# Performance work log

Hardware: AMD Instinct MI355X
Metric: run time of the kernel (lower is better)

## Reference

```python
import jax, jax.numpy as jnp
import numpy as np
import math

N_HEAD = 16
DEG = 2
EPS = 1e-7


def setup_inputs() -> dict:
    key = jax.random.key(0)
    k1, k2 = jax.random.split(key)
    B, T, C = 2, 2048, 1024
    x = jax.random.normal(k1, (B, T, C), dtype=jnp.float32)
    W = jax.random.normal(k2, (3 * C + N_HEAD, C), dtype=jnp.float32) * (1.0 / math.sqrt(C))
    return {"x": x, "W": W}


def reference(x, W):
    # JacobAttentionLayer.forward with attention_kernel='powerref' (AttentionReference,
    # deg=2, scale=1/sqrt(hs), eps=1e-7, log-space power softmax, gating=True).
    B, T, C = x.shape
    nh = N_HEAD
    hs = C // nh
    scale = 1.0 / math.sqrt(hs)

    qkvgr = jnp.einsum('btc,oc->bto', x, W)  # [B,T,3C+nh]
    q, k, v = (qkvgr[..., :C], qkvgr[..., C:2 * C], qkvgr[..., 2 * C:3 * C])
    log_g = jax.nn.log_sigmoid(qkvgr[..., 3 * C:].astype(jnp.float32))  # [B,T,nh]
    log_G = jnp.cumsum(log_g, axis=1).transpose(0, 2, 1)  # [B,nh,T]

    def heads(a):  # [B,T,C] -> [B,nh,T,hs]
        return a.reshape(B, T, nh, hs).transpose(0, 2, 1, 3)

    Q, K, V = heads(q), heads(k), heads(v)

    S = jnp.einsum('bhtd,bhsd->bhts', Q, K)  # [B,nh,T,T]
    # log-space power attention: deg*log(|S|+eps) + log(scale) + gating
    Tm = DEG * jnp.log(jnp.abs(S) + EPS) + jnp.log(jnp.float32(scale))
    Z = Tm + log_G[..., :, None] - log_G[..., None, :]
    mask = jnp.tril(jnp.ones((T, T), dtype=bool))
    Z = jnp.where(mask, Z, -jnp.inf)
    Z_rowmax = jax.lax.stop_gradient(jnp.max(Z, axis=-1, keepdims=True))
    P = jnp.exp(Z - Z_rowmax)  # deg even -> no sign correction

    norm = jnp.sum(P, axis=-1)  # [B,nh,T]
    O = jnp.einsum('bhts,bhsd->bhtd', P, V)
    y = O / norm[..., None]
    return y.transpose(0, 2, 1, 3).reshape(B, T, C)
```

## Files before the change

### kernel.cpp

```cpp
#include <hip/hip_runtime.h>
#include <math.h>

typedef __attribute__((ext_vector_type(4))) float f32x4;
typedef __attribute__((ext_vector_type(8))) short short8;

#define NEG_INF (-__builtin_inff())

__device__ __forceinline__ unsigned short f2bf(float f) {
    union { float f; unsigned u; } v; v.f = f;
    unsigned r = v.u + 0x7FFFu + ((v.u >> 16) & 1u);
    return (unsigned short)(r >> 16);
}
__device__ __forceinline__ float bf2f(unsigned short h) {
    union { unsigned u; float f; } v; v.u = ((unsigned)h) << 16;
    return v.f;
}

__device__ __forceinline__ f32x4 mfma_bf16(short8 a, short8 b, f32x4 c) {
    return __builtin_amdgcn_mfma_f32_16x16x32_bf16(a, b, c, 0, 0, 0);
}

__device__ __forceinline__ void gload_lds16(const unsigned short* g, unsigned short* l) {
    __builtin_amdgcn_global_load_lds(
        (const __attribute__((address_space(1))) void*)g,
        (__attribute__((address_space(3))) void*)l, 16, 0, 0);
}

__global__ void split_kernel(const float* __restrict__ in,
                             unsigned short* __restrict__ hi,
                             unsigned short* __restrict__ lo, int n4)
{
    int i = blockIdx.x * 256 + threadIdx.x;
    if (i >= n4) return;
    float4 v = ((const float4*)in)[i];
    ushort4 h, l;
    h.x = f2bf(v.x); l.x = f2bf(v.x - bf2f(h.x));
    h.y = f2bf(v.y); l.y = f2bf(v.y - bf2f(h.y));
    h.z = f2bf(v.z); l.z = f2bf(v.z - bf2f(h.z));
    h.w = f2bf(v.w); l.w = f2bf(v.w - bf2f(h.w));
    ((ushort4*)hi)[i] = h;
    ((ushort4*)lo)[i] = l;
}

__global__ __launch_bounds__(256, 3)
void gemm_proj(const unsigned short* __restrict__ xh, const unsigned short* __restrict__ xl,
               const unsigned short* __restrict__ wh, const unsigned short* __restrict__ wl,
               unsigned short* __restrict__ Qh, unsigned short* __restrict__ Ql,
               unsigned short* __restrict__ Kh, unsigned short* __restrict__ Kl,
               unsigned short* __restrict__ Vtg, float* __restrict__ gbuf)
{
    __shared__ __align__(16) unsigned short Ah[128][32];
    __shared__ __align__(16) unsigned short Al[128][32];
    __shared__ __align__(16) unsigned short Bh[128][32];
    __shared__ __align__(16) unsigned short Bl[128][32];

    const int mt = blockIdx.x & 31;
    const int nt = blockIdx.x >> 5;
    const int m0 = mt * 128, n0 = nt * 128;
    const int tid = threadIdx.x;
    const int w = tid >> 6, l = tid & 63;
    const int wm = w >> 1, wn = w & 1;
    const int lr = l & 15, lq = l >> 4;
    const int xs = (lr >> 1) & 3;
    const bool needLo = (nt < 16) || (nt == 24);

    f32x4 acc[4][4];
#pragma unroll
    for (int i = 0; i < 4; ++i)
#pragma unroll
        for (int j = 0; j < 4; ++j) acc[i][j] = (f32x4){0.f, 0.f, 0.f, 0.f};

    const int srow = tid >> 2;
    const int sp = tid & 3;

    for (int k0 = 0; k0 < 1024; k0 += 32) {
        __syncthreads();
#pragma unroll
        for (int p = 0; p < 2; ++p) {
            int r = srow + p * 64;
            int sc = (sp ^ ((r >> 1) & 3)) * 8;
            int o = n0 + r;
            int oc = o < 3088 ? o : 3087;
            gload_lds16(&xh[(size_t)(m0 + r) * 1024 + k0 + sc], &Ah[r][sp * 8]);
            gload_lds16(&wh[(size_t)oc * 1024 + k0 + sc],       &Bh[r][sp * 8]);
            if (needLo) {
                gload_lds16(&xl[(size_t)(m0 + r) * 1024 + k0 + sc], &Al[r][sp * 8]);
                gload_lds16(&wl[(size_t)oc * 1024 + k0 + sc],       &Bl[r][sp * 8]);
            }
        }
        __asm__ volatile("s_waitcnt vmcnt(0)" ::: "memory");
        __syncthreads();

        short8 ah[4], bh4[4], al4[4], bl4[4];
#pragma unroll
        for (int i = 0; i < 4; ++i) {
            ah[i]  = *(const short8*)&Ah[wm * 64 + i * 16 + lr][(lq ^ xs) * 8];
            bh4[i] = *(const short8*)&Bh[wn * 64 + i * 16 + lr][(lq ^ xs) * 8];
        }
        if (needLo) {
#pragma unroll
            for (int i = 0; i < 4; ++i) {
                al4[i] = *(const short8*)&Al[wm * 64 + i * 16 + lr][(lq ^ xs) * 8];
                bl4[i] = *(const short8*)&Bl[wn * 64 + i * 16 + lr][(lq ^ xs) * 8];
            }
        }
#pragma unroll
        for (int i = 0; i < 4; ++i)
#pragma unroll
            for (int j = 0; j < 4; ++j) {
                acc[i][j] = mfma_bf16(ah[i], bh4[j], acc[i][j]);
                if (needLo) {
                    acc[i][j] = mfma_bf16(ah[i], bl4[j], acc[i][j]);
                    acc[i][j] = mfma_bf16(al4[i], bh4[j], acc[i][j]);
                }
            }
    }

#pragma unroll
    for (int i = 0; i < 4; ++i) {
        int nrow0 = m0 + wm * 64 + i * 16 + lq * 4;
        int b = nrow0 >> 11;
        int tbase = nrow0 & 2047;
#pragma unroll
        for (int j = 0; j < 4; ++j) {
            int o = n0 + wn * 64 + j * 16 + lr;
            if (o < 1024) {
                int h = o >> 6, d = o & 63;
                size_t base = ((size_t)(b * 16 + h) * 2048 + tbase) * 64 + d;
#pragma unroll
                for (int r = 0; r < 4; ++r) {
                    float v = acc[i][j][r];
                    unsigned short hi_ = f2bf(v);
                    unsigned short lo_ = f2bf(v - bf2f(hi_));
                    Qh[base + (size_t)r * 64] = hi_;
                    Ql[base + (size_t)r * 64] = lo_;
                }
            } else if (o < 2048) {
                int oo = o - 1024;
                int h = oo >> 6, d = oo & 63;
                size_t base = ((size_t)(b * 16 + h) * 2048 + tbase) * 64 + d;
#pragma unroll
                for (int r = 0; r < 4; ++r) {
                    float v = acc[i][j][r];
                    unsigned short hi_ = f2bf(v);
                    unsigned short lo_ = f2bf(v - bf2f(hi_));
                    Kh[base + (size_t)r * 64] = hi_;
                    Kl[base + (size_t)r * 64] = lo_;
                }
            } else if (o < 3072) {
                int oo = o - 2048;
                int h = oo >> 6, d = oo & 63;
                size_t base = ((size_t)(b * 16 + h) * 64 + d) * 2048 + tbase;
                ushort4 pk;
                pk.x = f2bf(acc[i][j][0]);
                pk.y = f2bf(acc[i][j][1]);
                pk.z = f2bf(acc[i][j][2]);
                pk.w = f2bf(acc[i][j][3]);
                *(ushort4*)&Vtg[base] = pk;
            } else if (o < 3088) {
                int og = o - 3072;
#pragma unroll
                for (int r = 0; r < 4; ++r)
                    gbuf[(size_t)(nrow0 + r) * 16 + og] = acc[i][j][r];
            }
        }
    }
}

__global__ void gate_scan(const float* __restrict__ g, float* __restrict__ lg)
{
    const int bh = blockIdx.x;
    const int b = bh >> 4, h = bh & 15;
    const int tid = threadIdx.x;
    __shared__ float part[256];

    float vals[8];
    float run = 0.f;
#pragma unroll
    for (int j = 0; j < 8; ++j) {
        int t = tid * 8 + j;
        float x = g[(size_t)(b * 2048 + t) * 16 + h];
        float ls = fminf(x, 0.f) - log1pf(__expf(-fabsf(x)));
        run += ls * 1.4426950408889634f;
        vals[j] = run;
    }
    part[tid] = run;
    __syncthreads();
    for (int ofs = 1; ofs < 256; ofs <<= 1) {
        float add = (tid >= ofs) ? part[tid - ofs] : 0.f;
        __syncthreads();
        part[tid] += add;
        __syncthreads();
    }
    float excl = part[tid] - run;
#pragma unroll
    for (int j = 0; j < 8; ++j)
        lg[(size_t)bh * 2048 + tid * 8 + j] = excl + vals[j];
}

__global__ __launch_bounds__(256, 3)
void attn_fwd(const unsigned short* __restrict__ Qh, const unsigned short* __restrict__ Ql,
              const unsigned short* __restrict__ Kh, const unsigned short* __restrict__ Kl,
              const unsigned short* __restrict__ Vtg, const float* __restrict__ lg,
              float* __restrict__ out)
{
    __shared__ __align__(16) unsigned short kh[64][64];
    __shared__ __align__(16) unsigned short kl[64][64];
    __shared__ __align__(16) unsigned short vs[64][64];
    __shared__ __align__(16) unsigned short pl[4][16][64];

    const int bid = blockIdx.x;
    const int qi = (bid & 7) | ((bid >> 8) << 3);
    const int bh = (bid >> 3) & 31;
    const int tid = threadIdx.x;
    const int w = tid >> 6, l = tid & 63;
    const int lr = l & 15, lq = l >> 4;
    const int xk = lr & 7;
    const int q0 = qi * 64;
    const int myrow0 = q0 + w * 16;

    const size_t qoff = ((size_t)bh * 2048 + myrow0 + lr) * 64;
    short8 qh8[2], ql8[2];
    qh8[0] = *(const short8*)&Qh[qoff + lq * 8];
    qh8[1] = *(const short8*)&Qh[qoff + 32 + lq * 8];
    ql8[0] = *(const short8*)&Ql[qoff + lq * 8];
    ql8[1] = *(const short8*)&Ql[qoff + 32 + lq * 8];

    float gq2[4];
#pragma unroll
    for (int r = 0; r < 4; ++r)
        gq2[r] = lg[(size_t)bh * 2048 + myrow0 + lq * 4 + r] - 3.0f;

    float M_[4]  = {0.f, 0.f, 0.f, 0.f};
    float ls_[4] = {0.f, 0.f, 0.f, 0.f};
    f32x4 o4[4];
#pragma unroll
    for (int i = 0; i < 4; ++i) o4[i] = (f32x4){0.f, 0.f, 0.f, 0.f};

    const int srow = tid >> 3;
    const int schunk = tid & 7;

    const unsigned short* Kh_b = Kh + (size_t)bh * 2048 * 64;
    const unsigned short* Kl_b = Kl + (size_t)bh * 2048 * 64;
    const unsigned short* Vt_b = Vtg + (size_t)bh * 64 * 2048;

    for (int kv0 = 0; kv0 <= q0; kv0 += 64) {
        __syncthreads();
#pragma unroll
        for (int p = 0; p < 2; ++p) {
            int r = srow + p * 32;
            int sc = (schunk ^ (r & 7)) * 8;
            gload_lds16(&Kh_b[(size_t)(kv0 + r) * 64 + sc], &kh[r][schunk * 8]);
            gload_lds16(&Kl_b[(size_t)(kv0 + r) * 64 + sc], &kl[r][schunk * 8]);
            gload_lds16(&Vt_b[(size_t)r * 2048 + kv0 + sc], &vs[r][schunk * 8]);
        }
        __asm__ volatile("s_waitcnt vmcnt(0)" ::: "memory");
        __syncthreads();

        float gsl[4];
#pragma unroll
        for (int js = 0; js < 4; ++js)
            gsl[js] = lg[(size_t)bh * 2048 + kv0 + js * 16 + lr];

        f32x4 sa[4];
#pragma unroll
        for (int js = 0; js < 4; ++js) sa[js] = (f32x4){0.f, 0.f, 0.f, 0.f};
#pragma unroll
        for (int js = 0; js < 4; ++js)
#pragma unroll
            for (int ks = 0; ks < 2; ++ks) {
                short8 kb  = *(const short8*)&kh[js * 16 + lr][((ks * 4 + lq) ^ xk) << 3];
                short8 kbl = *(const short8*)&kl[js * 16 + lr][((ks * 4 + lq) ^ xk) << 3];
                sa[js] = mfma_bf16(qh8[ks], kb,  sa[js]);
                sa[js] = mfma_bf16(qh8[ks], kbl, sa[js]);
                sa[js] = mfma_bf16(ql8[ks], kb,  sa[js]);
            }

        const bool diag = (kv0 == q0);
#pragma unroll
        for (int js = 0; js < 4; ++js) {
            float ga = gsl[js];
#pragma unroll
            for (int r = 0; r < 4; ++r) {
                float a = fabsf(sa[js][r]) + 1e-7f;
                float ex = exp2f(gq2[r] - ga);
                float wv = a * a * ex;
                if (diag && (js * 16 + lr > w * 16 + lq * 4 + r)) wv = 0.f;
                sa[js][r] = wv;
            }
        }

        float f_[4], rMv[4];
#pragma unroll
        for (int r = 0; r < 4; ++r) {
            float a = fmaxf(fmaxf(sa[0][r], sa[1][r]), fmaxf(sa[2][r], sa[3][r]));
#pragma unroll
            for (int msk = 1; msk < 16; msk <<= 1)
                a = fmaxf(a, __shfl_xor(a, msk, 16));
            float Mn = fmaxf(M_[r], a);
            bool pos = Mn > 1e-30f;
            float rM = pos ? __builtin_amdgcn_rcpf(Mn) : 0.f;
            f_[r]  = pos ? M_[r] * rM : 1.f;
            rMv[r] = rM;
            M_[r]  = Mn;
        }

        float rs_[4] = {0.f, 0.f, 0.f, 0.f};
#pragma unroll
        for (int js = 0; js < 4; ++js)
#pragma unroll
            for (int r = 0; r < 4; ++r) {
                float pv = sa[js][r] * rMv[r];
                sa[js][r] = pv;
                rs_[r] += pv;
            }
#pragma unroll
        for (int r = 0; r < 4; ++r) {
            float s = rs_[r];
#pragma unroll
            for (int msk = 1; msk < 16; msk <<= 1)
                s += __shfl_xor(s, msk, 16);
            ls_[r] = ls_[r] * f_[r] + s;
        }
#pragma unroll
        for (int ds_ = 0; ds_ < 4; ++ds_)
#pragma unroll
            for (int r = 0; r < 4; ++r)
                o4[ds_][r] *= f_[r];

#pragma unroll
        for (int js = 0; js < 4; ++js)
#pragma unroll
            for (int r = 0; r < 4; ++r) {
                int prow = lq * 4 + r;
                int cch = (js * 2 + (lr >> 3)) ^ (prow & 7);
                pl[w][prow][(cch << 3) | (lr & 7)] = f2bf(sa[js][r]);
            }
        __asm__ volatile("s_waitcnt lgkmcnt(0)" ::: "memory");
        __builtin_amdgcn_sched_barrier(0);

        short8 pa0 = *(const short8*)&pl[w][lr][((0 + lq) ^ xk) << 3];
        short8 pa1 = *(const short8*)&pl[w][lr][((4 + lq) ^ xk) << 3];
#pragma unroll
        for (int ds_ = 0; ds_ < 4; ++ds_) {
            short8 vb0 = *(const short8*)&vs[ds_ * 16 + lr][((0 + lq) ^ xk) << 3];
            short8 vb1 = *(const short8*)&vs[ds_ * 16 + lr][((4 + lq) ^ xk) << 3];
            o4[ds_] = mfma_bf16(pa0, vb0, o4[ds_]);
            o4[ds_] = mfma_bf16(pa1, vb1, o4[ds_]);
        }
    }

    const int b = bh >> 4, h = bh & 15;
#pragma unroll
    for (int ds_ = 0; ds_ < 4; ++ds_)
#pragma unroll
        for (int r = 0; r < 4; ++r) {
            int t = myrow0 + lq * 4 + r;
            out[(size_t)(b * 2048 + t) * 1024 + h * 64 + ds_ * 16 + lr] =
                o4[ds_][r] / ls_[r];
        }
}

extern "C" void kernel_launch(void* const* d_in, const int* in_sizes, int n_in,
                              void* d_out, int out_size, void* d_ws, size_t ws_size,
                              hipStream_t stream)
{
    const float* x = (const float*)d_in[0];
    const float* W = (const float*)d_in[1];
    float* out = (float*)d_out;

    const size_t NX = 4194304;
    const size_t NW = 3162112;
    const size_t NQ = 4194304;

    char* ws = (char*)d_ws;
    size_t off = 0;
    auto alloc = [&](size_t bytes) -> void* {
        void* p = ws + off;
        off += (bytes + 255) & ~(size_t)255;
        return p;
    };
    unsigned short* xh = (unsigned short*)alloc(NX * 2);
    unsigned short* xl = (unsigned short*)alloc(NX * 2);
    unsigned short* wh = (unsigned short*)alloc(NW * 2);
    unsigned short* wl = (unsigned short*)alloc(NW * 2);
    unsigned short* Qh = (unsigned short*)alloc(NQ * 2);
    unsigned short* Ql = (unsigned short*)alloc(NQ * 2);
    unsigned short* Kh = (unsigned short*)alloc(NQ * 2);
    unsigned short* Kl = (unsigned short*)alloc(NQ * 2);
    unsigned short* Vt = (unsigned short*)alloc(NQ * 2);
    float* g  = (float*)alloc(65536 * 4);
    float* lg = (float*)alloc(65536 * 4);
    if (off > ws_size) return;

    split_kernel<<<(int)(NX / 4 + 255) / 256, 256, 0, stream>>>(x, xh, xl, (int)(NX / 4));
    split_kernel<<<(int)(NW / 4 + 255) / 256, 256, 0, stream>>>(W, wh, wl, (int)(NW / 4));
    gemm_proj<<<800, 256, 0, stream>>>(xh, xl, wh, wl, Qh, Ql, Kh, Kl, Vt, g);
    gate_scan<<<32, 256, 0, stream>>>(g, lg);
    attn_fwd<<<1024, 256, 0, stream>>>(Qh, Ql, Kh, Kl, Vt, lg, out);
}
```

Before: 213.6 us.

## Double-buffer LDS tiles in projection GEMM and attention, reverse KV order with lazy rescale

Both the projection GEMM and the attention kernel now use two LDS buffers, so the global-to-LDS load of the next tile is issued before computing on the current one. This hides memory latency behind MFMA work. The attention kernel also walks KV tiles from the diagonal backwards and skips the running-max rescale of the output and normaliser unless some row's max grows. The cost is twice the shared memory and occupancy lowered from 3 to 2 blocks per CU.

```diff
diff --git a/kernel.cpp b/kernel.cpp
--- a/kernel.cpp
+++ b/kernel.cpp
@@ -42,17 +42,17 @@
     ((ushort4*)lo)[i] = l;
 }
 
-__global__ __launch_bounds__(256, 3)
+__global__ __launch_bounds__(256, 2)
 void gemm_proj(const unsigned short* __restrict__ xh, const unsigned short* __restrict__ xl,
                const unsigned short* __restrict__ wh, const unsigned short* __restrict__ wl,
                unsigned short* __restrict__ Qh, unsigned short* __restrict__ Ql,
                unsigned short* __restrict__ Kh, unsigned short* __restrict__ Kl,
                unsigned short* __restrict__ Vtg, float* __restrict__ gbuf)
 {
-    __shared__ __align__(16) unsigned short Ah[128][32];
-    __shared__ __align__(16) unsigned short Al[128][32];
-    __shared__ __align__(16) unsigned short Bh[128][32];
-    __shared__ __align__(16) unsigned short Bl[128][32];
+    __shared__ __align__(16) unsigned short Ah[2][128][32];
+    __shared__ __align__(16) unsigned short Al[2][128][32];
+    __shared__ __align__(16) unsigned short Bh[2][128][32];
+    __shared__ __align__(16) unsigned short Bl[2][128][32];
 
     const int mt = blockIdx.x & 31;
     const int nt = blockIdx.x >> 5;
@@ -73,35 +73,41 @@
     const int srow = tid >> 2;
     const int sp = tid & 3;
 
-    for (int k0 = 0; k0 < 1024; k0 += 32) {
-        __syncthreads();
+    auto STAGE = [&](int bsel, int k0) {
 #pragma unroll
         for (int p = 0; p < 2; ++p) {
             int r = srow + p * 64;
             int sc = (sp ^ ((r >> 1) & 3)) * 8;
             int o = n0 + r;
             int oc = o < 3088 ? o : 3087;
-            gload_lds16(&xh[(size_t)(m0 + r) * 1024 + k0 + sc], &Ah[r][sp * 8]);
-            gload_lds16(&wh[(size_t)oc * 1024 + k0 + sc],       &Bh[r][sp * 8]);
+            gload_lds16(&xh[(size_t)(m0 + r) * 1024 + k0 + sc], &Ah[bsel][r][sp * 8]);
+            gload_lds16(&wh[(size_t)oc * 1024 + k0 + sc],       &Bh[bsel][r][sp * 8]);
             if (needLo) {
-                gload_lds16(&xl[(size_t)(m0 + r) * 1024 + k0 + sc], &Al[r][sp * 8]);
-                gload_lds16(&wl[(size_t)oc * 1024 + k0 + sc],       &Bl[r][sp * 8]);
-            }
-        }
-        __asm__ volatile("s_waitcnt vmcnt(0)" ::: "memory");
-        __syncthreads();
+                gload_lds16(&xl[(size_t)(m0 + r) * 1024 + k0 + sc], &Al[bsel][r][sp * 8]);
+                gload_lds16(&wl[(size_t)oc * 1024 + k0 + sc],       &Bl[bsel][r][sp * 8]);
+            }
+        }
+    };
+
+    STAGE(0, 0);
+    __asm__ volatile("s_waitcnt vmcnt(0)" ::: "memory");
+    __syncthreads();
+
+    int cur = 0;
+    for (int k0 = 0; k0 < 1024; k0 += 32) {
+        if (k0 + 32 < 1024) STAGE(cur ^ 1, k0 + 32);
 
         short8 ah[4], bh4[4], al4[4], bl4[4];
 #pragma unroll
         for (int i = 0; i < 4; ++i) {
-            ah[i]  = *(const short8*)&Ah[wm * 64 + i * 16 + lr][(lq ^ xs) * 8];
-            bh4[i] = *(const short8*)&Bh[wn * 64 + i * 16 + lr][(lq ^ xs) * 8];
+            ah[i]  = *(const short8*)&Ah[cur][wm * 64 + i * 16 + lr][(lq ^ xs) * 8];
+            bh4[i] = *(const short8*)&Bh[cur][wn * 64 + i * 16 + lr][(lq ^ xs) * 8];
         }
         if (needLo) {
 #pragma unroll
             for (int i = 0; i < 4; ++i) {
-                al4[i] = *(const short8*)&Al[wm * 64 + i * 16 + lr][(lq ^ xs) * 8];
-                bl4[i] = *(const short8*)&Bl[wn * 64 + i * 16 + lr][(lq ^ xs) * 8];
+                al4[i] = *(const short8*)&Al[cur][wm * 64 + i * 16 + lr][(lq ^ xs) * 8];
+                bl4[i] = *(const short8*)&Bl[cur][wn * 64 + i * 16 + lr][(lq ^ xs) * 8];
             }
         }
 #pragma unroll
@@ -114,6 +120,10 @@
                     acc[i][j] = mfma_bf16(al4[i], bh4[j], acc[i][j]);
                 }
             }
+
+        __asm__ volatile("s_waitcnt vmcnt(0)" ::: "memory");
+        __syncthreads();
+        cur ^= 1;
     }
 
 #pragma unroll
@@ -198,15 +208,15 @@
         lg[(size_t)bh * 2048 + tid * 8 + j] = excl + vals[j];
 }
 
-__global__ __launch_bounds__(256, 3)
+__global__ __launch_bounds__(256, 2)
 void attn_fwd(const unsigned short* __restrict__ Qh, const unsigned short* __restrict__ Ql,
               const unsigned short* __restrict__ Kh, const unsigned short* __restrict__ Kl,
               const unsigned short* __restrict__ Vtg, const float* __restrict__ lg,
               float* __restrict__ out)
 {
-    __shared__ __align__(16) unsigned short kh[64][64];
-    __shared__ __align__(16) unsigned short kl[64][64];
-    __shared__ __align__(16) unsigned short vs[64][64];
+    __shared__ __align__(16) unsigned short kh[2][64][64];
+    __shared__ __align__(16) unsigned short kl[2][64][64];
+    __shared__ __align__(16) unsigned short vs[2][64][64];
     __shared__ __align__(16) unsigned short pl[4][16][64];
 
     const int bid = blockIdx.x;
@@ -233,6 +243,7 @@
 
     float M_[4]  = {0.f, 0.f, 0.f, 0.f};
     float ls_[4] = {0.f, 0.f, 0.f, 0.f};
+    float rMv[4] = {0.f, 0.f, 0.f, 0.f};
     f32x4 o4[4];
 #pragma unroll
     for (int i = 0; i < 4; ++i) o4[i] = (f32x4){0.f, 0.f, 0.f, 0.f};
@@ -244,18 +255,25 @@
     const unsigned short* Kl_b = Kl + (size_t)bh * 2048 * 64;
     const unsigned short* Vt_b = Vtg + (size_t)bh * 64 * 2048;
 
-    for (int kv0 = 0; kv0 <= q0; kv0 += 64) {
-        __syncthreads();
+    auto STAGE = [&](int bsel, int kv0) {
 #pragma unroll
         for (int p = 0; p < 2; ++p) {
             int r = srow + p * 32;
             int sc = (schunk ^ (r & 7)) * 8;
-            gload_lds16(&Kh_b[(size_t)(kv0 + r) * 64 + sc], &kh[r][schunk * 8]);
-            gload_lds16(&Kl_b[(size_t)(kv0 + r) * 64 + sc], &kl[r][schunk * 8]);
-            gload_lds16(&Vt_b[(size_t)r * 2048 + kv0 + sc], &vs[r][schunk * 8]);
-        }
-        __asm__ volatile("s_waitcnt vmcnt(0)" ::: "memory");
-        __syncthreads();
+            gload_lds16(&Kh_b[(size_t)(kv0 + r) * 64 + sc], &kh[bsel][r][schunk * 8]);
+            gload_lds16(&Kl_b[(size_t)(kv0 + r) * 64 + sc], &kl[bsel][r][schunk * 8]);
+            gload_lds16(&Vt_b[(size_t)r * 2048 + kv0 + sc], &vs[bsel][r][schunk * 8]);
+        }
+    };
+
+    STAGE(0, q0);
+    __asm__ volatile("s_waitcnt vmcnt(0)" ::: "memory");
+    __syncthreads();
+
+    int cur = 0;
+    for (int it = 0; it <= qi; ++it) {
+        const int kv0 = q0 - (it << 6);
+        if (it < qi) STAGE(cur ^ 1, kv0 - 64);
 
         float gsl[4];
 #pragma unroll
@@ -269,14 +287,14 @@
         for (int js = 0; js < 4; ++js)
 #pragma unroll
             for (int ks = 0; ks < 2; ++ks) {
-                short8 kb  = *(const short8*)&kh[js * 16 + lr][((ks * 4 + lq) ^ xk) << 3];
-                short8 kbl = *(const short8*)&kl[js * 16 + lr][((ks * 4 + lq) ^ xk) << 3];
+                short8 kb  = *(const short8*)&kh[cur][js * 16 + lr][((ks * 4 + lq) ^ xk) << 3];
+                short8 kbl = *(const short8*)&kl[cur][js * 16 + lr][((ks * 4 + lq) ^ xk) << 3];
                 sa[js] = mfma_bf16(qh8[ks], kb,  sa[js]);
                 sa[js] = mfma_bf16(qh8[ks], kbl, sa[js]);
                 sa[js] = mfma_bf16(ql8[ks], kb,  sa[js]);
             }
 
-        const bool diag = (kv0 == q0);
+        const bool diag = (it == 0);
 #pragma unroll
         for (int js = 0; js < 4; ++js) {
             float ga = gsl[js];
@@ -290,19 +308,28 @@
             }
         }
 
-        float f_[4], rMv[4];
+        float a4[4];
 #pragma unroll
         for (int r = 0; r < 4; ++r) {
             float a = fmaxf(fmaxf(sa[0][r], sa[1][r]), fmaxf(sa[2][r], sa[3][r]));
 #pragma unroll
             for (int msk = 1; msk < 16; msk <<= 1)
                 a = fmaxf(a, __shfl_xor(a, msk, 16));
-            float Mn = fmaxf(M_[r], a);
-            bool pos = Mn > 1e-30f;
-            float rM = pos ? __builtin_amdgcn_rcpf(Mn) : 0.f;
-            f_[r]  = pos ? M_[r] * rM : 1.f;
-            rMv[r] = rM;
-            M_[r]  = Mn;
+            a4[r] = a;
+        }
+        int grow = (a4[0] > M_[0]) | (a4[1] > M_[1]) | (a4[2] > M_[2]) | (a4[3] > M_[3]);
+        if (__any(grow)) {
+#pragma unroll
+            for (int r = 0; r < 4; ++r) {
+                float Mn = fmaxf(M_[r], a4[r]);
+                float rM = (Mn > 1e-30f) ? __builtin_amdgcn_rcpf(Mn) : 0.f;
+                float f  = (a4[r] > M_[r]) ? M_[r] * rM : 1.f;
+                M_[r] = Mn;
+                rMv[r] = rM;
+                ls_[r] *= f;
+#pragma unroll
+                for (int ds_ = 0; ds_ < 4; ++ds_) o4[ds_][r] *= f;
+            }
         }
 
         float rs_[4] = {0.f, 0.f, 0.f, 0.f};
@@ -320,13 +347,8 @@
 #pragma unroll
             for (int msk = 1; msk < 16; msk <<= 1)
                 s += __shfl_xor(s, msk, 16);
-            ls_[r] = ls_[r] * f_[r] + s;
-        }
-#pragma unroll
-        for (int ds_ = 0; ds_ < 4; ++ds_)
-#pragma unroll
-            for (int r = 0; r < 4; ++r)
-                o4[ds_][r] *= f_[r];
+            ls_[r] += s;
+        }
 
 #pragma unroll
         for (int js = 0; js < 4; ++js)
@@ -343,11 +365,15 @@
         short8 pa1 = *(const short8*)&pl[w][lr][((4 + lq) ^ xk) << 3];
 #pragma unroll
         for (int ds_ = 0; ds_ < 4; ++ds_) {
-            short8 vb0 = *(const short8*)&vs[ds_ * 16 + lr][((0 + lq) ^ xk) << 3];
-            short8 vb1 = *(const short8*)&vs[ds_ * 16 + lr][((4 + lq) ^ xk) << 3];
+            short8 vb0 = *(const short8*)&vs[cur][ds_ * 16 + lr][((0 + lq) ^ xk) << 3];
+            short8 vb1 = *(const short8*)&vs[cur][ds_ * 16 + lr][((4 + lq) ^ xk) << 3];
             o4[ds_] = mfma_bf16(pa0, vb0, o4[ds_]);
             o4[ds_] = mfma_bf16(pa1, vb1, o4[ds_]);
         }
+
+        __asm__ volatile("s_waitcnt vmcnt(0)" ::: "memory");
+        __syncthreads();
+        cur ^= 1;
     }
 
     const int b = bh >> 4, h = bh & 15;
```

After: 231.4 us. +8.4%, slower.
